# Optimization experiments

Measured on AMD Instinct MI355X. Metric: run time of the kernel, lower is better.

The kernel has to match this reference:

```python
import jax, jax.numpy as jnp
import numpy as np

S = 24; N = S * S; D = 1024; B = 4; H = 8; HD = D // H; K = 8
LN_EPS = 1e-5


def _spiral_indices(s, clockwise):
    inds = []
    top, bottom, left, right = 0, s - 1, 0, s - 1
    if clockwise:
        while top <= bottom and left <= right:
            for j in range(left, right + 1):
                inds.append((top, j))
            top += 1
            for i in range(top, bottom + 1):
                inds.append((i, right))
            right -= 1
            if top <= bottom:
                for j in range(right, left - 1, -1):
                    inds.append((bottom, j))
                bottom -= 1
            if left <= right:
                for i in range(bottom, top - 1, -1):
                    inds.append((i, left))
                left += 1
    else:
        while top <= bottom and left <= right:
            for i in range(top, bottom + 1):
                inds.append((i, left))
            left += 1
            for j in range(left, right + 1):
                inds.append((bottom, j))
            bottom -= 1
            if left <= right:
                for i in range(bottom, top - 1, -1):
                    inds.append((i, right))
                right -= 1
            if top <= bottom:
                for j in range(right, left - 1, -1):
                    inds.append((top, j))
                top += 1
    return np.array([i * s + j for i, j in inds], dtype=np.int32)


def _diag_indices(s, anti):
    idx = []
    for offset in (range(2 * s - 1) if anti else range(-(s - 1), s)):
        for i in range(s):
            j = (offset - i) if anti else (i + offset)
            if 0 <= j < s:
                idx.append(i * s + j)
    return np.array(idx, dtype=np.int32)


def _build_scan_indices(s):
    # Composite (scan + restore) permutation per direction: out_i = Linear_i(x[:, idx_i])
    ar = np.arange(s * s, dtype=np.int32).reshape(s, s)
    lr = ar.reshape(-1)                      # left_right: identity
    rl_scan = ar[:, ::-1].reshape(-1)        # right_left scan
    rl_restore = ar[:, ::-1].reshape(-1)     # restore flips width back
    rl = rl_scan[rl_restore]                 # composes to identity
    tb = ar.T.reshape(-1)                    # top_bottom (restore is plain view -> no inverse!)
    bt_scan = ar[::-1, :].T.reshape(-1)      # bottom_top scan: flip(transpose) flatten
    bt_restore = ar[::-1, :].reshape(-1)     # restore: view->transpose->flip(2)->transpose
    bt = bt_scan[bt_restore]
    dm = _diag_indices(s, anti=False)        # restore is plain view
    da = _diag_indices(s, anti=True)
    sc = _spiral_indices(s, clockwise=True)
    scc = _spiral_indices(s, clockwise=False)
    return np.stack([lr, rl, tb, bt, dm, da, sc, scc], axis=0)  # [8, N]


def setup_inputs() -> dict:
    key = jax.random.key(0)
    ks = jax.random.split(key, 12)
    sc = D ** -0.5
    return {
        "vision_features": jax.random.normal(ks[0], (B, N, D), dtype=jnp.float32),
        "dir_W": jax.random.normal(ks[1], (K, D, D), dtype=jnp.float32) * sc,
        "dir_b": jax.random.normal(ks[2], (K, D), dtype=jnp.float32) * 0.01,
        "in_proj_w": jax.random.normal(ks[3], (3 * D, D), dtype=jnp.float32) * sc,
        "in_proj_b": jax.random.normal(ks[4], (3 * D,), dtype=jnp.float32) * 0.01,
        "out_proj_w": jax.random.normal(ks[5], (D, D), dtype=jnp.float32) * sc,
        "out_proj_b": jax.random.normal(ks[6], (D,), dtype=jnp.float32) * 0.01,
        "fin_w": jax.random.normal(ks[7], (D, D), dtype=jnp.float32) * sc,
        "fin_b": jax.random.normal(ks[8], (D,), dtype=jnp.float32) * 0.01,
        "ln_g": jnp.ones((D,), dtype=jnp.float32),
        "ln_b": jnp.zeros((D,), dtype=jnp.float32),
        "scan_idx": jnp.asarray(_build_scan_indices(S)),  # [8, N] int32
    }


def reference(vision_features, dir_W, dir_b, in_proj_w, in_proj_b,
              out_proj_w, out_proj_b, fin_w, fin_b, ln_g, ln_b, scan_idx):
    b, n, d = vision_features.shape
    # Fused per-direction gather + batched GEMM: [B,8,N,D]
    gathered = vision_features[:, scan_idx]                     # [B,K,N,D]
    dirs = jnp.einsum('bknd,kde->bkne', gathered, dir_W) + dir_b[None, :, None, :]
    kv = dirs.reshape(b, K * n, d)                              # [B,8N,D]
    # MultiheadAttention (batch_first, 8 heads, eval -> no dropout)
    wq, wk, wv = in_proj_w[:d], in_proj_w[d:2 * d], in_proj_w[2 * d:]
    bq, bk, bv = in_proj_b[:d], in_proj_b[d:2 * d], in_proj_b[2 * d:]
    q = (vision_features @ wq.T + bq).reshape(b, n, H, HD).transpose(0, 2, 1, 3)
    k = (kv @ wk.T + bk).reshape(b, K * n, H, HD).transpose(0, 2, 1, 3)
    v = (kv @ wv.T + bv).reshape(b, K * n, H, HD).transpose(0, 2, 1, 3)
    scores = jnp.einsum('bhnd,bhmd->bhnm', q, k) / jnp.sqrt(jnp.asarray(HD, q.dtype))
    attn = jax.nn.softmax(scores, axis=-1)
    o = jnp.einsum('bhnm,bhmd->bhnd', attn, v).transpose(0, 2, 1, 3).reshape(b, n, d)
    fused = o @ out_proj_w.T + out_proj_b
    # output_projection: Linear -> LayerNorm (dropout inactive)
    y = fused @ fin_w.T + fin_b
    mu = jnp.mean(y, axis=-1, keepdims=True)
    var = jnp.mean(jnp.square(y - mu), axis=-1, keepdims=True)
    y = (y - mu) * jax.lax.rsqrt(var + LN_EPS) * ln_g + ln_b
    return y + vision_features
```

## Files before the change

kernel.cpp:

```cpp
#include <hip/hip_runtime.h>
#include <hip/hip_bf16.h>

typedef __attribute__((ext_vector_type(8))) short short8;
typedef __attribute__((ext_vector_type(4))) short short4v;
typedef __attribute__((ext_vector_type(4))) float f32x4;
typedef __attribute__((ext_vector_type(4))) int i32x4;

#define NTOK 576
#define DIM  1024
#define NB   4
#define NH   8
#define HD   128
#define KDIR 8
#define KN   4608
#define NSPLIT 4
#define NT 18

__device__ __forceinline__ float us2f(unsigned short u) {
    unsigned int x = ((unsigned int)u) << 16;
    return __uint_as_float(x);
}
__device__ __forceinline__ unsigned short f2us(float f) {
    unsigned int x = __float_as_uint(f);
    unsigned int r = x + 0x7fffu + ((x >> 16) & 1u);
    return (unsigned short)(r >> 16);
}

typedef __attribute__((address_space(3))) unsigned int lds_uint;
typedef const __attribute__((address_space(1))) unsigned int glb_uint;
__device__ __forceinline__ void async16(const unsigned short* g, unsigned short* l) {
    __builtin_amdgcn_global_load_lds((glb_uint*)g, (lds_uint*)l, 16, 0, 0);
}
__device__ __forceinline__ void wait_vm0_barrier() {
    asm volatile("s_waitcnt vmcnt(0)" ::: "memory");
    __builtin_amdgcn_s_barrier();
    __builtin_amdgcn_sched_barrier(0);
}

__global__ void detect_kernel(const unsigned int* __restrict__ src, int* meta)
{
    if (threadIdx.x == 0) {
        int cnt = 0;
        for (int i = 0; i < 256; ++i) {
            unsigned u = src[(long)i * 16384] & 0xFFFFu;
            unsigned e = (u >> 7) & 0xFFu;
            cnt += (e >= 90 && e <= 150) ? 1 : 0;
        }
        meta[0] = (cnt >= 192) ? 1 : 0;
    }
}

struct ConvJobs {
    const void* src[10];
    unsigned short* dst[10];
    int n4[10];
    int bstart[10];
};
__global__ __launch_bounds__(256)
void conv_all(ConvJobs J, const int* __restrict__ meta)
{
    const int b = blockIdx.x;
    int ji = 0;
    #pragma unroll
    for (int i = 1; i < 10; ++i) if (b >= J.bstart[i]) ji = i;
    const long base = (long)(b - J.bstart[ji]) * 1024 + threadIdx.x;
    const long n4 = J.n4[ji];
    if (meta[0]) {
        const ushort4* s = (const ushort4*)J.src[ji];
        ushort4* d = (ushort4*)J.dst[ji];
        #pragma unroll
        for (int t = 0; t < 4; ++t) {
            long i = base + t * 256;
            if (i < n4) d[i] = s[i];
        }
    } else {
        const float4* s = (const float4*)J.src[ji];
        ushort4* d = (ushort4*)J.dst[ji];
        #pragma unroll
        for (int t = 0; t < 4; ++t) {
            long i = base + t * 256;
            if (i < n4) {
                float4 v = s[i];
                ushort4 o;
                o.x = f2us(v.x); o.y = f2us(v.y); o.z = f2us(v.z); o.w = f2us(v.w);
                d[i] = o;
            }
        }
    }
}

__global__ __launch_bounds__(256)
void transpose_conv(const void* __restrict__ src, unsigned short* __restrict__ dst,
                    const int* __restrict__ meta)
{
    const int k = blockIdx.y;
    const int ty = blockIdx.x >> 5, tx = blockIdx.x & 31;
    const int d0 = ty * 32, e0 = tx * 32;
    __shared__ float tl[32][33];
    const int t = threadIdx.x;
    const int row = t >> 3, c4 = (t & 7) * 4;
    const long sbase = ((long)k * 1024 + d0 + row) * 1024 + e0 + c4;
    if (meta[0]) {
        const unsigned short* s = (const unsigned short*)src;
        ushort4 v = *(const ushort4*)(s + sbase);
        tl[row][c4+0] = us2f(v.x); tl[row][c4+1] = us2f(v.y);
        tl[row][c4+2] = us2f(v.z); tl[row][c4+3] = us2f(v.w);
    } else {
        const float* s = (const float*)src;
        float4 v = *(const float4*)(s + sbase);
        tl[row][c4+0] = v.x; tl[row][c4+1] = v.y;
        tl[row][c4+2] = v.z; tl[row][c4+3] = v.w;
    }
    __syncthreads();
    ushort4 o;
    o.x = f2us(tl[c4+0][row]); o.y = f2us(tl[c4+1][row]);
    o.z = f2us(tl[c4+2][row]); o.w = f2us(tl[c4+3][row]);
    *(ushort4*)(dst + ((long)k * 1024 + e0 + row) * 1024 + d0 + c4) = o;
}

template<int MODE, int TN, int BM, int BN>
__global__ __launch_bounds__(256)
void gemm_glds(const unsigned short* __restrict__ A, const unsigned short* __restrict__ Bw,
               const unsigned short* __restrict__ bias, unsigned short* __restrict__ C,
               const unsigned short* __restrict__ B2, const unsigned short* __restrict__ bias2,
               unsigned short* __restrict__ C2,
               int M, long bStride, long biasStride)
{
    constexpr int MI = BM / 32, NI = BN / 32;
    const int z = blockIdx.y;
    const unsigned short* Bb;
    const unsigned short* Gb;
    if constexpr (MODE == 6) {
        Bb = (z < 8) ? Bw + (long)z * bStride : B2;
        Gb = (z < 8) ? bias + (long)z * biasStride : bias2;
    } else {
        Bb = Bw + (long)z * bStride;
        Gb = bias + (long)z * biasStride;
    }
    const int tm = blockIdx.x / TN;
    const int tn = blockIdx.x % TN;

    __shared__ __align__(16) unsigned short As[2][BM * 64];
    __shared__ __align__(16) unsigned short Bs[2][BN * 64];

    const int tid = threadIdx.x, lane = tid & 63, wid = tid >> 6;
    const int wm = wid >> 1, wn = wid & 1;
    const int r0 = lane & 15, hi = lane >> 4;
    const int lr = lane >> 3;
    const int lg = lane & 7;

    f32x4 zz = {0.f, 0.f, 0.f, 0.f};
    f32x4 acc[MI][NI];
    #pragma unroll
    for (int i = 0; i < MI; ++i)
        #pragma unroll
        for (int j = 0; j < NI; ++j) acc[i][j] = zz;

    const int sgc = ((lg ^ (lr & 7)) << 3);

    auto stage = [&](int k0, int buf) {
        #pragma unroll
        for (int j = 0; j < BM / 32; ++j) {
            int rb = wid * (BM / 4) + j * 8;
            async16(A + (long)(tm * BM + rb + lr) * 1024 + k0 + sgc, &As[buf][rb * 64]);
        }
        #pragma unroll
        for (int j = 0; j < BN / 32; ++j) {
            int rb = wid * (BN / 4) + j * 8;
            async16(Bb + (long)(tn * BN + rb + lr) * 1024 + k0 + sgc, &Bs[buf][rb * 64]);
        }
    };

    stage(0, 0);
    for (int kt = 0; kt < 16; ++kt) {
        wait_vm0_barrier();
        if (kt < 15) stage((kt + 1) * 64, (kt + 1) & 1);
        const unsigned short* Asb = As[kt & 1];
        const unsigned short* Bsb = Bs[kt & 1];
        __builtin_amdgcn_s_setprio(1);
        #pragma unroll
        for (int kd = 0; kd < 2; ++kd) {
            const int pg = ((kd * 4 + hi) ^ (r0 & 7)) << 3;
            short8 af[MI], bfr[NI];
            #pragma unroll
            for (int mi = 0; mi < MI; ++mi)
                af[mi] = *reinterpret_cast<const short8*>(&Asb[(wm * (BM/2) + mi * 16 + r0) * 64 + pg]);
            #pragma unroll
            for (int ni = 0; ni < NI; ++ni)
                bfr[ni] = *reinterpret_cast<const short8*>(&Bsb[(wn * (BN/2) + ni * 16 + r0) * 64 + pg]);
            #pragma unroll
            for (int mi = 0; mi < MI; ++mi)
                #pragma unroll
                for (int ni = 0; ni < NI; ++ni)
                    acc[mi][ni] = __builtin_amdgcn_mfma_f32_16x16x32_bf16(af[mi], bfr[ni], acc[mi][ni], 0, 0, 0);
        }
        __builtin_amdgcn_s_setprio(0);
    }

    const float QSCL = 0.08838834764831845f * 1.4426950408889634f;
    const int jr = hi * 4;
    #pragma unroll
    for (int ni = 0; ni < NI; ++ni) {
        int cg = tn * BN + wn * (BN/2) + ni * 16 + r0;
        float bv = us2f(Gb[cg]);
        if constexpr (MODE == 5) {
            if (cg >= 1024) {
                int cg2 = cg - 1024;
                int h = cg2 >> 7, d = cg2 & 127;
                #pragma unroll
                for (int mi = 0; mi < MI; ++mi) {
                    int rgb = tm * BM + wm * (BM/2) + mi * 16 + jr;
                    int b = rgb / 4608, kv = rgb - b * 4608;
                    ushort4 o;
                    o.x = f2us(acc[mi][ni][0] + bv);
                    o.y = f2us(acc[mi][ni][1] + bv);
                    o.z = f2us(acc[mi][ni][2] + bv);
                    o.w = f2us(acc[mi][ni][3] + bv);
                    *(ushort4*)&C2[((long)(b * 8 + h) * 128 + d) * 4608 + kv] = o;
                }
                continue;
            }
        }
        #pragma unroll
        for (int mi = 0; mi < MI; ++mi) {
            #pragma unroll
            for (int j = 0; j < 4; ++j) {
                int rg = tm * BM + wm * (BM/2) + mi * 16 + jr + j;
                float val = acc[mi][ni][j] + bv;
                if constexpr (MODE == 0) {
                    C[(long)rg * 1024 + cg] = f2us(val);
                } else if constexpr (MODE == 5) {
                    int b = rg / 4608, kv = rg - b * 4608;
                    int h = cg >> 7, d = cg & 127;
                    C[((long)(b * 8 + h) * 4608 + kv) * 128 + d] = f2us(val);
                } else {
                    int b = rg / 576, n = rg - b * 576;
                    if (z == 8) {
                        int h = cg >> 7, d = cg & 127;
                        C2[((long)(b * 8 + h) * 576 + n) * 128 + d] = f2us(val * QSCL);
                    } else {
                        C[((long)b * 4608 + (long)z * 576 + n) * 1024 + cg] = f2us(val);
                    }
                }
            }
        }
    }
}

__global__ __launch_bounds__(256)
void attn_kernel6(const unsigned short* __restrict__ Qh, const unsigned short* __restrict__ Kh,
                  const unsigned short* __restrict__ VTh, unsigned short* __restrict__ Opart,
                  float2* __restrict__ Ml)
{
    const int bid = blockIdx.x;
    const int logical = (bid & 7) * 144 + (bid >> 3);
    const int bhsp = logical / 9;
    const int qt = logical - bhsp * 9;
    const int bh = bhsp >> 2;
    const int sp = bhsp & 3;

    const int tid = threadIdx.x;
    const int lane = tid & 63, wid = tid >> 6;
    const int r0 = lane & 15, hi = lane >> 4;
    const int k8 = hi * 8;

    __shared__ __align__(16) unsigned short Ks[2][64 * 128];
    __shared__ __align__(16) unsigned short VT[2][128 * 64];

    short8 qf[4];
    {
        const long qoff = ((long)bh * NTOK + qt * 64 + wid * 16 + r0) * HD;
        #pragma unroll
        for (int kd = 0; kd < 4; ++kd)
            qf[kd] = *reinterpret_cast<const short8*>(Qh + qoff + kd * 32 + k8);
    }

    f32x4 zz = {0.f, 0.f, 0.f, 0.f};
    f32x4 oacc[8];
    #pragma unroll
    for (int i = 0; i < 8; ++i) oacc[i] = zz;
    float mrun = -1e30f, lrun = 0.f;

    int offK[4], offV[4];
    #pragma unroll
    for (int j = 0; j < 4; ++j) {
        offK[j] = (wid * 16 + 4 * j + hi) * 128 + (((lane & 15) ^ ((4 * j + hi) & 7)) << 3);
        offV[j] = (wid * 32 + 8 * j + (lane >> 3)) * KN + (((lane & 7) ^ (lane >> 3)) << 3);
    }
    const unsigned short* kp = Kh + (long)bh * KN * HD + (long)(sp * (KN / NSPLIT)) * HD;
    const unsigned short* vp = VTh + (long)bh * HD * KN + sp * (KN / NSPLIT);

    auto stage = [&](int buf) {
        #pragma unroll
        for (int j = 0; j < 4; ++j) {
            async16(kp + offK[j], &Ks[buf][(wid * 16 + 4 * j) * 128]);
            async16(vp + offV[j], &VT[buf][(wid * 32 + 8 * j) * 64]);
        }
    };

    stage(0);
    for (int kt = 0; kt < NT; ++kt) {
        wait_vm0_barrier();
        if (kt < NT - 1) { kp += 64 * HD; vp += 64; stage((kt + 1) & 1); }
        const unsigned short* Ksb = Ks[kt & 1];
        const unsigned short* VTb = VT[kt & 1];

        f32x4 s[4];
        #pragma unroll
        for (int nb = 0; nb < 4; ++nb) s[nb] = zz;
        __builtin_amdgcn_s_setprio(1);
        #pragma unroll
        for (int nb = 0; nb < 4; ++nb) {
            const int krow = nb * 16 + r0;
            #pragma unroll
            for (int kd = 0; kd < 4; ++kd) {
                short8 kf = *reinterpret_cast<const short8*>(
                    &Ksb[krow * 128 + (((kd * 4 + hi) ^ (r0 & 7)) << 3)]);
                s[nb] = __builtin_amdgcn_mfma_f32_16x16x32_bf16(kf, qf[kd], s[nb], 0, 0, 0);
            }
        }
        __builtin_amdgcn_s_setprio(0);

        float mt = fmaxf(fmaxf(fmaxf(s[0][0], s[0][1]), fmaxf(s[0][2], s[0][3])),
                   fmaxf(fmaxf(fmaxf(s[1][0], s[1][1]), fmaxf(s[1][2], s[1][3])),
                   fmaxf(fmaxf(fmaxf(s[2][0], s[2][1]), fmaxf(s[2][2], s[2][3])),
                         fmaxf(fmaxf(s[3][0], s[3][1]), fmaxf(s[3][2], s[3][3])))));
        if (!__all(mt - mrun <= 8.0f)) {
            float mr = fmaxf(mt, __shfl_xor(mt, 16));
            mr = fmaxf(mr, __shfl_xor(mr, 32));
            float mn = fmaxf(mrun, mr);
            float scl = exp2f(mrun - mn);
            mrun = mn;
            lrun *= scl;
            #pragma unroll
            for (int db = 0; db < 8; ++db)
                #pragma unroll
                for (int j = 0; j < 4; ++j)
                    oacc[db][j] *= scl;
        }
        float p[4][4];
        float rt = 0.f;
        #pragma unroll
        for (int nb = 0; nb < 4; ++nb)
            #pragma unroll
            for (int j = 0; j < 4; ++j) {
                p[nb][j] = exp2f(s[nb][j] - mrun);
                rt += p[nb][j];
            }
        lrun += rt;

        unsigned pk0[4], pk1[4];
        #pragma unroll
        for (int nb = 0; nb < 4; ++nb) {
            asm("v_cvt_pk_bf16_f32 %0, %1, %2" : "=v"(pk0[nb]) : "v"(p[nb][0]), "v"(p[nb][1]));
            asm("v_cvt_pk_bf16_f32 %0, %1, %2" : "=v"(pk1[nb]) : "v"(p[nb][2]), "v"(p[nb][3]));
        }

        __builtin_amdgcn_s_setprio(1);
        #pragma unroll
        for (int kd = 0; kd < 2; ++kd) {
            i32x4 fr;
            fr[0] = (int)pk0[2 * kd];
            fr[1] = (int)pk1[2 * kd];
            fr[2] = (int)pk0[2 * kd + 1];
            fr[3] = (int)pk1[2 * kd + 1];
            short8 pf = *reinterpret_cast<short8*>(&fr);
            const int cg0 = (hi >> 1) + 4 * kd;
            const int sub = (hi & 1) << 2;
            #pragma unroll
            for (int db = 0; db < 8; ++db) {
                const int vrow = (db * 16 + r0) * 64;
                short4v lo = *(const short4v*)&VTb[vrow + ((cg0 ^ (r0 & 7)) << 3) + sub];
                short4v hh = *(const short4v*)&VTb[vrow + (((cg0 + 2) ^ (r0 & 7)) << 3) + sub];
                short8 vf = {lo[0], lo[1], lo[2], lo[3], hh[0], hh[1], hh[2], hh[3]};
                oacc[db] = __builtin_amdgcn_mfma_f32_16x16x32_bf16(vf, pf, oacc[db], 0, 0, 0);
            }
        }
        __builtin_amdgcn_s_setprio(0);
    }

    lrun += __shfl_xor(lrun, 16);
    lrun += __shfl_xor(lrun, 32);
    const float inv = 1.f / lrun;
    const long po = ((long)(sp * 32 + bh) * NTOK + qt * 64 + wid * 16 + r0) * HD;
    #pragma unroll
    for (int db = 0; db < 8; ++db) {
        ushort4 o;
        o.x = f2us(oacc[db][0] * inv);
        o.y = f2us(oacc[db][1] * inv);
        o.z = f2us(oacc[db][2] * inv);
        o.w = f2us(oacc[db][3] * inv);
        *(ushort4*)&Opart[po + db * 16 + hi * 4] = o;
    }
    if (lane < 16) {
        const long mo = (long)(sp * 32 + bh) * NTOK + qt * 64 + wid * 16 + r0;
        Ml[mo] = make_float2(mrun, lrun);
    }
}

__global__ __launch_bounds__(256)
void attn_reduce(const unsigned short* __restrict__ Opart, const float2* __restrict__ Ml,
                 unsigned short* __restrict__ Ob)
{
    const int qt = blockIdx.x, bh = blockIdx.y;
    const int t = threadIdx.x;
    const int rl = t >> 2, dc = (t & 3) * 32;
    const int q = qt * 64 + rl;

    float m[NSPLIT], l[NSPLIT];
    float M = -1e30f;
    #pragma unroll
    for (int sp = 0; sp < NSPLIT; ++sp) {
        float2 v = Ml[(long)(sp * 32 + bh) * NTOK + q];
        m[sp] = v.x; l[sp] = v.y;
        M = fmaxf(M, v.x);
    }
    float w[NSPLIT], denom = 0.f;
    #pragma unroll
    for (int sp = 0; sp < NSPLIT; ++sp) {
        w[sp] = l[sp] * exp2f(m[sp] - M);
        denom += w[sp];
    }
    const float inv = 1.f / denom;
    const int b = bh >> 3, h = bh & 7;
    #pragma unroll
    for (int dj = 0; dj < 4; ++dj) {
        float a[8];
        #pragma unroll
        for (int e = 0; e < 8; ++e) a[e] = 0.f;
        #pragma unroll
        for (int sp = 0; sp < NSPLIT; ++sp) {
            short8 v = *reinterpret_cast<const short8*>(
                &Opart[((long)(sp * 32 + bh) * NTOK + q) * HD + dc + dj * 8]);
            #pragma unroll
            for (int e = 0; e < 8; ++e)
                a[e] += w[sp] * us2f((unsigned short)v[e]);
        }
        short8 o;
        #pragma unroll
        for (int e = 0; e < 8; ++e) o[e] = (short)f2us(a[e] * inv);
        *reinterpret_cast<short8*>(&Ob[((long)b * NTOK + q) * 1024 + h * 128 + dc + dj * 8]) = o;
    }
}

__global__ __launch_bounds__(256)
void ln2_kernel(const unsigned short* __restrict__ Y, const unsigned short* __restrict__ g,
                const unsigned short* __restrict__ be, const unsigned short* __restrict__ vis,
                void* __restrict__ dout, const int* __restrict__ meta)
{
    const int row = blockIdx.x;
    const int tid = threadIdx.x;
    const int lane = tid & 63, wid = tid >> 6;
    const unsigned short* yr = Y + (long)row * DIM;
    ushort4 raw = reinterpret_cast<const ushort4*>(yr)[tid];
    float v[4];
    v[0] = us2f(raw.x); v[1] = us2f(raw.y); v[2] = us2f(raw.z); v[3] = us2f(raw.w);
    float s1 = 0.f, s2 = 0.f;
    #pragma unroll
    for (int i = 0; i < 4; ++i) { s1 += v[i]; s2 += v[i] * v[i]; }
    #pragma unroll
    for (int off = 1; off < 64; off <<= 1) {
        s1 += __shfl_xor(s1, off);
        s2 += __shfl_xor(s2, off);
    }
    __shared__ float red[2][4];
    if (lane == 0) { red[0][wid] = s1; red[1][wid] = s2; }
    __syncthreads();
    s1 = red[0][0] + red[0][1] + red[0][2] + red[0][3];
    s2 = red[1][0] + red[1][1] + red[1][2] + red[1][3];
    const float mu = s1 * (1.f / DIM);
    const float var = s2 * (1.f / DIM) - mu * mu;
    const float inv = rsqrtf(var + 1e-5f);
    ushort4 gg = reinterpret_cast<const ushort4*>(g)[tid];
    ushort4 bb = reinterpret_cast<const ushort4*>(be)[tid];
    ushort4 vv = reinterpret_cast<const ushort4*>(vis + (long)row * DIM)[tid];
    float o0 = (v[0] - mu) * inv * us2f(gg.x) + us2f(bb.x) + us2f(vv.x);
    float o1 = (v[1] - mu) * inv * us2f(gg.y) + us2f(bb.y) + us2f(vv.y);
    float o2 = (v[2] - mu) * inv * us2f(gg.z) + us2f(bb.z) + us2f(vv.z);
    float o3 = (v[3] - mu) * inv * us2f(gg.w) + us2f(bb.w) + us2f(vv.w);
    if (meta[0]) {
        ushort4 o;
        o.x = f2us(o0); o.y = f2us(o1); o.z = f2us(o2); o.w = f2us(o3);
        reinterpret_cast<ushort4*>((unsigned short*)dout + (long)row * DIM)[tid] = o;
    } else {
        float4 o = make_float4(o0, o1, o2, o3);
        reinterpret_cast<float4*>((float*)dout + (long)row * DIM)[tid] = o;
    }
}

extern "C" void kernel_launch(void* const* d_in, const int* in_sizes, int n_in,
                              void* d_out, int out_size, void* d_ws, size_t ws_size,
                              hipStream_t stream)
{
    unsigned long long w = (unsigned long long)d_ws;
    int* meta = (int*)w; w += 256;

    const int cidx[10] = {0, 2, 3, 4, 5, 6, 7, 8, 9, 10};
    const long csz[10] = {
        (long)NB * NTOK * DIM,
        (long)KDIR * DIM,
        3L * DIM * DIM,
        3L * DIM,
        (long)DIM * DIM,
        DIM,
        (long)DIM * DIM,
        DIM, DIM, DIM
    };
    unsigned short* cv[10];
    for (int i = 0; i < 10; ++i) {
        cv[i] = (unsigned short*)w;
        w += (csz[i] * 2 + 255) & ~255ULL;
    }
    unsigned short* dWT = (unsigned short*)w; w += (long)KDIR * DIM * DIM * 2;

    const size_t big = (size_t)NB * KDIR * NTOK * DIM * 2;
    const size_t sml = (size_t)NB * NTOK * DIM * 2;
    unsigned short* dirs = (unsigned short*)w; w += big;
    unsigned short* Kh   = (unsigned short*)w; w += big;
    unsigned short* VTh  = (unsigned short*)w; w += big;
    unsigned short* Qh   = (unsigned short*)w; w += sml;
    unsigned short* Ob   = (unsigned short*)w; w += sml;
    unsigned short* Fu   = (unsigned short*)w; w += sml;
    unsigned short* Y2   = (unsigned short*)w; w += sml;
    float2* Ml = (float2*)w; w += (long)NSPLIT * 32 * NTOK * sizeof(float2);
    unsigned short* Opart = dirs;

    const unsigned short* vision = cv[0];
    const unsigned short* dirb = cv[1];
    const unsigned short* inW = cv[2];
    const unsigned short* inB = cv[3];
    const unsigned short* outW = cv[4];
    const unsigned short* outB = cv[5];
    const unsigned short* finW = cv[6];
    const unsigned short* finB = cv[7];
    const unsigned short* lng = cv[8];
    const unsigned short* lnbt = cv[9];

    dim3 blk(256, 1, 1);

    detect_kernel<<<dim3(1), dim3(64), 0, stream>>>((const unsigned int*)d_in[1], meta);

    ConvJobs J;
    int bacc = 0;
    for (int i = 0; i < 10; ++i) {
        J.src[i] = d_in[cidx[i]];
        J.dst[i] = cv[i];
        J.n4[i] = (int)(csz[i] / 4);
        J.bstart[i] = bacc;
        bacc += (int)((csz[i] / 4 + 1023) / 1024);
    }
    conv_all<<<dim3(bacc), blk, 0, stream>>>(J, meta);
    transpose_conv<<<dim3(1024, KDIR), blk, 0, stream>>>(d_in[1], dWT, meta);

    gemm_glds<6, 8, 128, 128><<<dim3(18 * 8, 9), blk, 0, stream>>>(
        vision, dWT, dirb, dirs, inW, inB, Qh, NB * NTOK, (long)DIM * DIM, DIM);

    gemm_glds<5, 16, 128, 128><<<dim3(144 * 16, 1), blk, 0, stream>>>(
        dirs, inW + DIM * DIM, inB + DIM, Kh, nullptr, nullptr, VTh, NB * KN, 0L, 0L);

    attn_kernel6<<<dim3(9 * 32 * NSPLIT), blk, 0, stream>>>(Qh, Kh, VTh, Opart, Ml);

    attn_reduce<<<dim3(9, 32), blk, 0, stream>>>(Opart, Ml, Ob);

    gemm_glds<0, 16, 64, 64><<<dim3(36 * 16, 1), blk, 0, stream>>>(
        Ob, outW, outB, Fu, nullptr, nullptr, nullptr, NB * NTOK, 0L, 0L);

    gemm_glds<0, 16, 64, 64><<<dim3(36 * 16, 1), blk, 0, stream>>>(
        Fu, finW, finB, Y2, nullptr, nullptr, nullptr, NB * NTOK, 0L, 0L);

    ln2_kernel<<<dim3(NB * NTOK), blk, 0, stream>>>(Y2, lng, lnbt, vision, d_out, meta);
}
```

Before: 389.7 us.

## Process three query tiles per attention block and permute V layout for 16B reads

New measurement: 346.2 us. 1.13x faster.

```diff
diff --git a/kernel.cpp b/kernel.cpp
--- a/kernel.cpp
+++ b/kernel.cpp
@@ -2,7 +2,6 @@
 #include <hip/hip_bf16.h>
 
 typedef __attribute__((ext_vector_type(8))) short short8;
-typedef __attribute__((ext_vector_type(4))) short short4v;
 typedef __attribute__((ext_vector_type(4))) float f32x4;
 typedef __attribute__((ext_vector_type(4))) int i32x4;
 
@@ -13,8 +12,8 @@
 #define HD   128
 #define KDIR 8
 #define KN   4608
-#define NSPLIT 4
-#define NT 18
+#define NSPLIT 8
+#define NT 9
 
 __device__ __forceinline__ float us2f(unsigned short u) {
     unsigned int x = ((unsigned int)u) << 16;
@@ -211,12 +210,15 @@
                 for (int mi = 0; mi < MI; ++mi) {
                     int rgb = tm * BM + wm * (BM/2) + mi * 16 + jr;
                     int b = rgb / 4608, kv = rgb - b * 4608;
+                    int r = kv & 63;
+                    int P = ((r >> 5) & 1) * 32 + ((r >> 3) & 1) * 16 + ((r >> 2) & 1) * 8
+                          + ((r >> 4) & 1) * 4 + (r & 3);
                     ushort4 o;
                     o.x = f2us(acc[mi][ni][0] + bv);
                     o.y = f2us(acc[mi][ni][1] + bv);
                     o.z = f2us(acc[mi][ni][2] + bv);
                     o.w = f2us(acc[mi][ni][3] + bv);
-                    *(ushort4*)&C2[((long)(b * 8 + h) * 128 + d) * 4608 + kv] = o;
+                    *(ushort4*)&C2[((long)(b * 8 + h) * 128 + d) * 4608 + (kv & ~63) + P] = o;
                 }
                 continue;
             }
@@ -247,39 +249,43 @@
     }
 }
 
-__global__ __launch_bounds__(256)
-void attn_kernel6(const unsigned short* __restrict__ Qh, const unsigned short* __restrict__ Kh,
+__global__ __launch_bounds__(256, 2)
+void attn_kernel7(const unsigned short* __restrict__ Qh, const unsigned short* __restrict__ Kh,
                   const unsigned short* __restrict__ VTh, unsigned short* __restrict__ Opart,
                   float2* __restrict__ Ml)
 {
     const int bid = blockIdx.x;
-    const int logical = (bid & 7) * 144 + (bid >> 3);
-    const int bhsp = logical / 9;
-    const int qt = logical - bhsp * 9;
-    const int bh = bhsp >> 2;
-    const int sp = bhsp & 3;
+    const int logical = (bid & 7) * 96 + (bid >> 3);
+    const int bhsp = logical / 3;
+    const int qt = logical - bhsp * 3;
+    const int bh = bhsp >> 3;
+    const int sp = bhsp & 7;
 
     const int tid = threadIdx.x;
     const int lane = tid & 63, wid = tid >> 6;
     const int r0 = lane & 15, hi = lane >> 4;
-    const int k8 = hi * 8;
 
     __shared__ __align__(16) unsigned short Ks[2][64 * 128];
     __shared__ __align__(16) unsigned short VT[2][128 * 64];
 
-    short8 qf[4];
-    {
-        const long qoff = ((long)bh * NTOK + qt * 64 + wid * 16 + r0) * HD;
+    short8 qf[3][4];
+    #pragma unroll
+    for (int c = 0; c < 3; ++c) {
+        const long qoff = ((long)bh * NTOK + qt * 192 + c * 64 + wid * 16 + r0) * HD + hi * 8;
         #pragma unroll
         for (int kd = 0; kd < 4; ++kd)
-            qf[kd] = *reinterpret_cast<const short8*>(Qh + qoff + kd * 32 + k8);
+            qf[c][kd] = *reinterpret_cast<const short8*>(Qh + qoff + kd * 32);
     }
 
     f32x4 zz = {0.f, 0.f, 0.f, 0.f};
-    f32x4 oacc[8];
-    #pragma unroll
-    for (int i = 0; i < 8; ++i) oacc[i] = zz;
-    float mrun = -1e30f, lrun = 0.f;
+    f32x4 oacc[3][8];
+    #pragma unroll
+    for (int c = 0; c < 3; ++c)
+        #pragma unroll
+        for (int i = 0; i < 8; ++i) oacc[c][i] = zz;
+    float mrun[3], lrun[3];
+    #pragma unroll
+    for (int c = 0; c < 3; ++c) { mrun[c] = -1e30f; lrun[c] = 0.f; }
 
     int offK[4], offV[4];
     #pragma unroll
@@ -305,96 +311,106 @@
         const unsigned short* Ksb = Ks[kt & 1];
         const unsigned short* VTb = VT[kt & 1];
 
-        f32x4 s[4];
-        #pragma unroll
-        for (int nb = 0; nb < 4; ++nb) s[nb] = zz;
+        f32x4 s[3][4];
+        #pragma unroll
+        for (int c = 0; c < 3; ++c)
+            #pragma unroll
+            for (int nb = 0; nb < 4; ++nb) s[c][nb] = zz;
         __builtin_amdgcn_s_setprio(1);
         #pragma unroll
         for (int nb = 0; nb < 4; ++nb) {
-            const int krow = nb * 16 + r0;
             #pragma unroll
             for (int kd = 0; kd < 4; ++kd) {
                 short8 kf = *reinterpret_cast<const short8*>(
-                    &Ksb[krow * 128 + (((kd * 4 + hi) ^ (r0 & 7)) << 3)]);
-                s[nb] = __builtin_amdgcn_mfma_f32_16x16x32_bf16(kf, qf[kd], s[nb], 0, 0, 0);
+                    &Ksb[(nb * 16 + r0) * 128 + (((kd * 4 + hi) ^ (r0 & 7)) << 3)]);
+                s[0][nb] = __builtin_amdgcn_mfma_f32_16x16x32_bf16(kf, qf[0][kd], s[0][nb], 0, 0, 0);
+                s[1][nb] = __builtin_amdgcn_mfma_f32_16x16x32_bf16(kf, qf[1][kd], s[1][nb], 0, 0, 0);
+                s[2][nb] = __builtin_amdgcn_mfma_f32_16x16x32_bf16(kf, qf[2][kd], s[2][nb], 0, 0, 0);
             }
         }
         __builtin_amdgcn_s_setprio(0);
 
-        float mt = fmaxf(fmaxf(fmaxf(s[0][0], s[0][1]), fmaxf(s[0][2], s[0][3])),
-                   fmaxf(fmaxf(fmaxf(s[1][0], s[1][1]), fmaxf(s[1][2], s[1][3])),
-                   fmaxf(fmaxf(fmaxf(s[2][0], s[2][1]), fmaxf(s[2][2], s[2][3])),
-                         fmaxf(fmaxf(s[3][0], s[3][1]), fmaxf(s[3][2], s[3][3])))));
-        if (!__all(mt - mrun <= 8.0f)) {
-            float mr = fmaxf(mt, __shfl_xor(mt, 16));
-            mr = fmaxf(mr, __shfl_xor(mr, 32));
-            float mn = fmaxf(mrun, mr);
-            float scl = exp2f(mrun - mn);
-            mrun = mn;
-            lrun *= scl;
-            #pragma unroll
-            for (int db = 0; db < 8; ++db)
+        unsigned pk0[3][4], pk1[3][4];
+        #pragma unroll
+        for (int c = 0; c < 3; ++c) {
+            float mt = fmaxf(fmaxf(fmaxf(s[c][0][0], s[c][0][1]), fmaxf(s[c][0][2], s[c][0][3])),
+                       fmaxf(fmaxf(fmaxf(s[c][1][0], s[c][1][1]), fmaxf(s[c][1][2], s[c][1][3])),
+                       fmaxf(fmaxf(fmaxf(s[c][2][0], s[c][2][1]), fmaxf(s[c][2][2], s[c][2][3])),
+                             fmaxf(fmaxf(s[c][3][0], s[c][3][1]), fmaxf(s[c][3][2], s[c][3][3])))));
+            if (!__all(mt - mrun[c] <= 8.0f)) {
+                float mr = fmaxf(mt, __shfl_xor(mt, 16));
+                mr = fmaxf(mr, __shfl_xor(mr, 32));
+                float mn = fmaxf(mrun[c], mr);
+                float scl = exp2f(mrun[c] - mn);
+                mrun[c] = mn;
+                lrun[c] *= scl;
                 #pragma unroll
-                for (int j = 0; j < 4; ++j)
-                    oacc[db][j] *= scl;
-        }
-        float p[4][4];
-        float rt = 0.f;
-        #pragma unroll
-        for (int nb = 0; nb < 4; ++nb)
-            #pragma unroll
-            for (int j = 0; j < 4; ++j) {
-                p[nb][j] = exp2f(s[nb][j] - mrun);
-                rt += p[nb][j];
-            }
-        lrun += rt;
-
-        unsigned pk0[4], pk1[4];
-        #pragma unroll
-        for (int nb = 0; nb < 4; ++nb) {
-            asm("v_cvt_pk_bf16_f32 %0, %1, %2" : "=v"(pk0[nb]) : "v"(p[nb][0]), "v"(p[nb][1]));
-            asm("v_cvt_pk_bf16_f32 %0, %1, %2" : "=v"(pk1[nb]) : "v"(p[nb][2]), "v"(p[nb][3]));
+                for (int db = 0; db < 8; ++db)
+                    #pragma unroll
+                    for (int j = 0; j < 4; ++j)
+                        oacc[c][db][j] *= scl;
+            }
+            float rt = 0.f;
+            #pragma unroll
+            for (int nb = 0; nb < 4; ++nb)
+                #pragma unroll
+                for (int j = 0; j < 4; ++j) {
+                    s[c][nb][j] = exp2f(s[c][nb][j] - mrun[c]);
+                    rt += s[c][nb][j];
+                }
+            lrun[c] += rt;
+            #pragma unroll
+            for (int nb = 0; nb < 4; ++nb) {
+                asm("v_cvt_pk_bf16_f32 %0, %1, %2" : "=v"(pk0[c][nb]) : "v"(s[c][nb][0]), "v"(s[c][nb][1]));
+                asm("v_cvt_pk_bf16_f32 %0, %1, %2" : "=v"(pk1[c][nb]) : "v"(s[c][nb][2]), "v"(s[c][nb][3]));
+            }
         }
 
         __builtin_amdgcn_s_setprio(1);
         #pragma unroll
         for (int kd = 0; kd < 2; ++kd) {
-            i32x4 fr;
-            fr[0] = (int)pk0[2 * kd];
-            fr[1] = (int)pk1[2 * kd];
-            fr[2] = (int)pk0[2 * kd + 1];
-            fr[3] = (int)pk1[2 * kd + 1];
-            short8 pf = *reinterpret_cast<short8*>(&fr);
-            const int cg0 = (hi >> 1) + 4 * kd;
-            const int sub = (hi & 1) << 2;
+            short8 pf[3];
+            #pragma unroll
+            for (int c = 0; c < 3; ++c) {
+                i32x4 fr;
+                fr[0] = (int)pk0[c][2 * kd];
+                fr[1] = (int)pk1[c][2 * kd];
+                fr[2] = (int)pk0[c][2 * kd + 1];
+                fr[3] = (int)pk1[c][2 * kd + 1];
+                pf[c] = *reinterpret_cast<short8*>(&fr);
+            }
             #pragma unroll
             for (int db = 0; db < 8; ++db) {
-                const int vrow = (db * 16 + r0) * 64;
-                short4v lo = *(const short4v*)&VTb[vrow + ((cg0 ^ (r0 & 7)) << 3) + sub];
-                short4v hh = *(const short4v*)&VTb[vrow + (((cg0 + 2) ^ (r0 & 7)) << 3) + sub];
-                short8 vf = {lo[0], lo[1], lo[2], lo[3], hh[0], hh[1], hh[2], hh[3]};
-                oacc[db] = __builtin_amdgcn_mfma_f32_16x16x32_bf16(vf, pf, oacc[db], 0, 0, 0);
+                short8 vf = *reinterpret_cast<const short8*>(
+                    &VTb[(db * 16 + r0) * 64 + (((kd * 4 + hi) ^ (r0 & 7)) << 3)]);
+                oacc[0][db] = __builtin_amdgcn_mfma_f32_16x16x32_bf16(vf, pf[0], oacc[0][db], 0, 0, 0);
+                oacc[1][db] = __builtin_amdgcn_mfma_f32_16x16x32_bf16(vf, pf[1], oacc[1][db], 0, 0, 0);
+                oacc[2][db] = __builtin_amdgcn_mfma_f32_16x16x32_bf16(vf, pf[2], oacc[2][db], 0, 0, 0);
             }
         }
         __builtin_amdgcn_s_setprio(0);
     }
 
-    lrun += __shfl_xor(lrun, 16);
-    lrun += __shfl_xor(lrun, 32);
-    const float inv = 1.f / lrun;
-    const long po = ((long)(sp * 32 + bh) * NTOK + qt * 64 + wid * 16 + r0) * HD;
-    #pragma unroll
-    for (int db = 0; db < 8; ++db) {
-        ushort4 o;
-        o.x = f2us(oacc[db][0] * inv);
-        o.y = f2us(oacc[db][1] * inv);
-        o.z = f2us(oacc[db][2] * inv);
-        o.w = f2us(oacc[db][3] * inv);
-        *(ushort4*)&Opart[po + db * 16 + hi * 4] = o;
-    }
-    if (lane < 16) {
-        const long mo = (long)(sp * 32 + bh) * NTOK + qt * 64 + wid * 16 + r0;
-        Ml[mo] = make_float2(mrun, lrun);
+    #pragma unroll
+    for (int c = 0; c < 3; ++c) {
+        float lr = lrun[c];
+        lr += __shfl_xor(lr, 16);
+        lr += __shfl_xor(lr, 32);
+        const float inv = 1.f / lr;
+        const long po = ((long)(sp * 32 + bh) * NTOK + qt * 192 + c * 64 + wid * 16 + r0) * HD;
+        #pragma unroll
+        for (int db = 0; db < 8; ++db) {
+            ushort4 o;
+            o.x = f2us(oacc[c][db][0] * inv);
+            o.y = f2us(oacc[c][db][1] * inv);
+            o.z = f2us(oacc[c][db][2] * inv);
+            o.w = f2us(oacc[c][db][3] * inv);
+            *(ushort4*)&Opart[po + db * 16 + hi * 4] = o;
+        }
+        if (lane < 16) {
+            const long mo = (long)(sp * 32 + bh) * NTOK + qt * 192 + c * 64 + wid * 16 + r0;
+            Ml[mo] = make_float2(mrun[c], lr);
+        }
     }
 }
 
@@ -558,7 +574,7 @@
     gemm_glds<5, 16, 128, 128><<<dim3(144 * 16, 1), blk, 0, stream>>>(
         dirs, inW + DIM * DIM, inB + DIM, Kh, nullptr, nullptr, VTh, NB * KN, 0L, 0L);
 
-    attn_kernel6<<<dim3(9 * 32 * NSPLIT), blk, 0, stream>>>(Qh, Kh, VTh, Opart, Ml);
+    attn_kernel7<<<dim3(3 * 32 * NSPLIT), blk, 0, stream>>>(Qh, Kh, VTh, Opart, Ml);
 
     attn_reduce<<<dim3(9, 32), blk, 0, stream>>>(Opart, Ml, Ob);
 
```
